# Performance work log

Measured on AMD Instinct MI355X. Metric: run time of the kernel, lower is better.

The kernel has to match this reference:

```python
import jax, jax.numpy as jnp
import numpy as np

T, K, E, D, F = 2048, 6, 32, 2048, 1408   # tokens, top_k, routed experts, dim, moe_inter_dim
S = 2                                      # fused shared experts
C = T * K // E                             # exact per-expert capacity (balanced routing)


def _silu_and_mul(gu):
    # merged gate_up activation: silu(gate_half) * up_half
    g, u = jnp.split(gu, 2, axis=-1)
    return jax.nn.silu(g) * u


def setup_inputs() -> dict:
    key = jax.random.key(0)
    ks = jax.random.split(key, 7)
    x = jax.random.normal(ks[0], (T, D), dtype=jnp.float32)
    # balanced routing: every expert receives exactly C = T*K/E token-expert pairs
    indices = jax.random.permutation(ks[1], jnp.arange(T * K, dtype=jnp.int32) % E).reshape(T, K)
    weights = jax.random.uniform(ks[2], (T, K), dtype=jnp.float32)
    scale = 0.02
    w_gate_up = jax.random.normal(ks[3], (E, D, 2 * F), dtype=jnp.float32) * scale
    w_down = jax.random.normal(ks[4], (E, F, D), dtype=jnp.float32) * scale
    w_gate_up_shared = jax.random.normal(ks[5], (S, D, 2 * F), dtype=jnp.float32) * scale
    w_down_shared = jax.random.normal(ks[6], (S, F, D), dtype=jnp.float32) * scale
    return {"x": x, "weights": weights, "w_gate_up": w_gate_up, "w_down": w_down,
            "w_gate_up_shared": w_gate_up_shared, "w_down_shared": w_down_shared,
            "indices": indices}


def reference(x, weights, w_gate_up, w_down, w_gate_up_shared, w_down_shared, indices):
    # ---- dispatch: sort token-expert pairs by expert id (balanced -> exactly C per expert)
    flat_e = indices.reshape(-1)                       # [T*K]
    order = jnp.argsort(flat_e, stable=True)           # [T*K] pair ids grouped by expert
    tok = order // K                                   # source token of each sorted pair
    w_sorted = weights.reshape(-1)[order]              # routing weight of each sorted pair
    xg = x[tok].reshape(E, C, D)                       # gathered per-expert inputs
    # ---- routed experts: grouped gate_up GEMM -> silu_and_mul -> down GEMM
    act = _silu_and_mul(jnp.einsum('ecd,edf->ecf', xg, w_gate_up))   # [E, C, F]
    down = jnp.einsum('ecf,efd->ecd', act, w_down)                   # [E, C, D]
    # ---- combine: weighted scatter-add back to token order (y[idx] += out * weights[idx, top])
    y = jnp.zeros_like(x).at[tok].add(down.reshape(E * C, D) * w_sorted[:, None])
    # ---- fused shared experts: run on all tokens, added unweighted
    act_s = _silu_and_mul(jnp.einsum('td,sdf->stf', x, w_gate_up_shared))  # [S, T, F]
    y = y + jnp.einsum('stf,sfd->td', act_s, w_down_shared)
    return y
```

## Files before the change

kernel.cpp:

```cpp
#include <hip/hip_runtime.h>
#include <hip/hip_bf16.h>

#define TT 2048
#define KK 6
#define EE 32
#define DD 2048
#define FF 1408
#define SS 2
#define CC 384

typedef __bf16 bf16_t;
typedef __attribute__((ext_vector_type(8))) __bf16 bf16x8;
typedef __attribute__((ext_vector_type(4))) float f32x4;
typedef unsigned int u32;

#define AS1 __attribute__((address_space(1)))
#define AS3 __attribute__((address_space(3)))

__device__ __forceinline__ u32 f2bf(float f) {
    u32 u = __builtin_bit_cast(u32, f);
    return (u + 0x7fffu + ((u >> 16) & 1u)) >> 16;
}
__device__ __forceinline__ u32 pack2(float a, float b) {
    return f2bf(a) | (f2bf(b) << 16);
}
__device__ __forceinline__ float silu_mul(float g, float u) {
    return (g / (1.0f + __expf(-g))) * u;
}

__global__ void k_dispatch(const int* __restrict__ idx, int* __restrict__ counts,
                           int* __restrict__ tok, int* __restrict__ sop) {
    int p = blockIdx.x * 256 + threadIdx.x;
    if (p >= TT * KK) return;
    int e = idx[p];
    int pos = atomicAdd(&counts[e], 1);
    int slot = e * CC + pos;
    tok[slot] = p / KK;
    sop[p] = slot;
}

__global__ void k_gather(const float* __restrict__ x, const int* __restrict__ tok,
                         bf16_t* __restrict__ xall) {
    int row = blockIdx.x;
    int srow = (row < EE * CC) ? tok[row] : (row - EE * CC);
    const float* src = x + (size_t)srow * DD;
    bf16_t* dst = xall + (size_t)row * DD;
    int c0 = threadIdx.x * 8;
    float4 a = *(const float4*)(src + c0);
    float4 b = *(const float4*)(src + c0 + 4);
    uint4 o;
    o.x = pack2(a.x, a.y); o.y = pack2(a.z, a.w);
    o.z = pack2(b.x, b.y); o.w = pack2(b.z, b.w);
    *(uint4*)(dst + c0) = o;
}

#define BSR 44
template<bool FUSED>
__global__ __launch_bounds__(512, 4) void k_gemm_r(
    const bf16_t* __restrict__ Aall, const float* __restrict__ Br,
    bf16_t* __restrict__ Out, int Kdim, int Bstr, int Ostr, int NB)
{
    const int lin = blockIdx.x;
    const int xcd = lin & 7, jj = lin >> 3;
    const int e = xcd + 8 * (jj / NB);
    const int nblk = jj % NB;

    const bf16_t* A = Aall + (size_t)e * CC * Kdim;
    const float* Bbase = Br + (size_t)e * Kdim * Bstr;

    const int tid = threadIdx.x;
    const int lane = tid & 63, wid = tid >> 6;
    const int m_base = wid * 48;
    const int l15 = lane & 15, lq = lane >> 4;
    const int arow = tid >> 2, ac = tid & 3;
    const int bn = tid & 63, kq = tid >> 6;

    const float* bsrc;
    bf16_t* Cout;
    if (FUSED) {
        bsrc = Bbase + ((bn & 32) ? FF : 0) + nblk * 32 + (bn & 31);
        Cout = Out + (size_t)e * CC * Ostr + nblk * 32;
    } else {
        bsrc = Bbase + nblk * 64 + bn;
        Cout = Out + (size_t)e * CC * Ostr + nblk * 64;
    }

    __shared__ __align__(16) bf16_t As[2][384 * 32];
    __shared__ __align__(16) bf16_t Bs[2][64 * BSR];

    f32x4 acc[3][4] = {};
    const int ks = Kdim >> 5;

    auto stageA = [&](int kt, bf16_t* dst) {
        const int k0 = kt << 5;
        #pragma unroll
        for (int i = 0; i < 3; ++i) {
            const int row = i * 128 + arow;
            const int c = ac ^ (arow & 3);
            const bf16_t* g = A + (size_t)row * Kdim + (k0 + c * 8);
            AS3 u32* l = (AS3 u32*)(void*)(dst + (size_t)(i * 128 + wid * 16) * 32);
            __builtin_amdgcn_global_load_lds((const AS1 u32*)(const void*)g, l, 16, 0, 0);
        }
    };
    auto loadB = [&](int kt, float* v) {
        const float* sp = bsrc + (size_t)((kt << 5) + kq * 4) * Bstr;
        #pragma unroll
        for (int t = 0; t < 4; ++t) v[t] = sp[(size_t)t * Bstr];
    };
    auto writeB = [&](bf16_t* bbuf, const float* v) {
        uint2 w;
        w.x = pack2(v[0], v[1]); w.y = pack2(v[2], v[3]);
        *(uint2*)(bbuf + (size_t)bn * BSR + kq * 4) = w;
    };
    auto compute = [&](const bf16_t* abuf, const bf16_t* bbuf) {
        __builtin_amdgcn_s_setprio(1);
        bf16x8 bfr[4];
        #pragma unroll
        for (int j = 0; j < 4; ++j) {
            const int n_ds = FUSED ? ((j & 1) * 16 + (j >> 1) * 32) : (j * 16);
            bfr[j] = *(const bf16x8*)(bbuf + (size_t)(n_ds + l15) * BSR + lq * 8);
        }
        #pragma unroll
        for (int m = 0; m < 3; ++m) {
            const int row = m_base + m * 16 + l15;
            bf16x8 af = *(const bf16x8*)(abuf + (size_t)row * 32
                           + (size_t)((lq ^ (row & 3)) * 8));
            #pragma unroll
            for (int j = 0; j < 4; ++j)
                acc[m][j] = __builtin_amdgcn_mfma_f32_16x16x32_bf16(af, bfr[j], acc[m][j], 0, 0, 0);
        }
        __builtin_amdgcn_s_setprio(0);
    };

    float r0[4], r1[4], r2[4], r3[4];
    bf16_t* const As0 = &As[0][0];  bf16_t* const As1 = &As[1][0];
    bf16_t* const Bs0 = &Bs[0][0];  bf16_t* const Bs1 = &Bs[1][0];

    loadB(0, r0);
    asm volatile("s_waitcnt vmcnt(0)" ::: "memory");
    writeB(Bs0, r0);
    loadB(1, r1);
    loadB(2, r2);
    stageA(0, As0);
    loadB(3, r3);

#define R_ITER(T, RLOAD, RWRITE, ASC, ASN, BSC, BSN)                      \
    {                                                                     \
        const int tb = ((T) + 4 < ks) ? (T) + 4 : ks - 1;                 \
        loadB(tb, RLOAD);                                                 \
        asm volatile("s_waitcnt vmcnt(8)" ::: "memory");                  \
        asm volatile("s_waitcnt lgkmcnt(0)" ::: "memory");                \
        __builtin_amdgcn_s_barrier();                                     \
        const int tn = ((T) + 1 < ks) ? (T) + 1 : ks - 1;                 \
        stageA(tn, ASN);                                                  \
        compute(ASC, BSC);                                                \
        writeB(BSN, RWRITE);                                              \
    }

    for (int t = 0; t < ks; t += 4) {
        R_ITER(t + 0, r0, r1, As0, As1, Bs0, Bs1);
        R_ITER(t + 1, r1, r2, As1, As0, Bs1, Bs0);
        R_ITER(t + 2, r2, r3, As0, As1, Bs0, Bs1);
        R_ITER(t + 3, r3, r0, As1, As0, Bs1, Bs0);
    }
#undef R_ITER

    if (FUSED) {
        #pragma unroll
        for (int m = 0; m < 3; ++m)
            #pragma unroll
            for (int j = 0; j < 2; ++j) {
                const int n = j * 16 + l15;
                #pragma unroll
                for (int rr = 0; rr < 4; ++rr) {
                    const int mm = m_base + m * 16 + lq * 4 + rr;
                    Cout[(size_t)mm * Ostr + n] = (bf16_t)silu_mul(acc[m][j][rr], acc[m][j + 2][rr]);
                }
            }
    } else {
        #pragma unroll
        for (int m = 0; m < 3; ++m)
            #pragma unroll
            for (int j = 0; j < 4; ++j) {
                const int n = j * 16 + l15;
                #pragma unroll
                for (int rr = 0; rr < 4; ++rr) {
                    const int mm = m_base + m * 16 + lq * 4 + rr;
                    Cout[(size_t)mm * Ostr + n] = (bf16_t)acc[m][j][rr];
                }
            }
    }
}

#define BSTR 40
template<bool FUSED>
__global__ __launch_bounds__(256) void k_gemm_s(
    const bf16_t* __restrict__ Ash, const float* __restrict__ Bsh,
    bf16_t* __restrict__ Out, int Kdim, int Bstr, int Ostr, int ash_stride,
    int nkeys, int KQ, int NBs)
{
    const int b = blockIdx.x;
    const int xcd = b & 7, jj = b >> 3;
    const int m = jj / KQ, kqi = jj % KQ;
    const int key = kqi * 8 + xcd;
    if (key >= nkeys) return;
    const int s = key / NBs, nb = key % NBs;

    const bf16_t* A = Ash + ((size_t)s * ash_stride + (size_t)m * 128) * Kdim;
    const float* Bp = Bsh + (size_t)s * Kdim * Bstr;

    const int tid = threadIdx.x;
    const int lane = tid & 63, wid = tid >> 6;
    const int m_off = (wid >> 1) * 64, wn = wid & 1;
    const int l15 = lane & 15, lq = lane >> 4;
    const int arow = tid >> 2, ac = tid & 3;
    const int bn = tid & 127, kh = tid >> 7;

    const float* bsrc;
    bf16_t* Cout;
    if (FUSED) {
        bsrc = Bp + ((bn & 64) ? FF : 0) + nb * 64 + (bn & 63);
        Cout = Out + ((size_t)s * TT + (size_t)m * 128) * Ostr + nb * 64;
    } else {
        bsrc = Bp + nb * 128 + bn;
        Cout = Out + ((size_t)s * TT + (size_t)m * 128) * Ostr + nb * 128;
    }

    __shared__ __align__(16) bf16_t As[2][128 * 32];
    __shared__ __align__(16) bf16_t Bs[2][128 * BSTR];

    f32x4 acc[4][4] = {};
    const int ks = Kdim >> 5;

    auto stageA = [&](int kt, bf16_t* dst) {
        const int k0 = kt << 5;
        #pragma unroll
        for (int i = 0; i < 2; ++i) {
            const int row = i * 64 + arow;
            const int c = ac ^ (arow & 3);
            const bf16_t* g = A + (size_t)row * Kdim + (k0 + c * 8);
            AS3 u32* l = (AS3 u32*)(void*)(dst + (size_t)(i * 64 + wid * 16) * 32);
            __builtin_amdgcn_global_load_lds((const AS1 u32*)(const void*)g, l, 16, 0, 0);
        }
    };
    auto loadB = [&](int kt, float* v) {
        const float* sp = bsrc + (size_t)((kt << 5) + kh * 16) * Bstr;
        #pragma unroll
        for (int t = 0; t < 16; ++t) v[t] = sp[(size_t)t * Bstr];
    };
    auto writeB = [&](bf16_t* bbuf, const float* v) {
        u32 p[8];
        #pragma unroll
        for (int t = 0; t < 8; ++t) p[t] = pack2(v[2 * t], v[2 * t + 1]);
        uint4 w0, w1;
        w0.x = p[0]; w0.y = p[1]; w0.z = p[2]; w0.w = p[3];
        w1.x = p[4]; w1.y = p[5]; w1.z = p[6]; w1.w = p[7];
        *(uint4*)(bbuf + (size_t)bn * BSTR + kh * 16) = w0;
        *(uint4*)(bbuf + (size_t)bn * BSTR + kh * 16 + 8) = w1;
    };
    auto compute = [&](const bf16_t* abuf, const bf16_t* bbuf) {
        bf16x8 af[4], bfr[4];
        #pragma unroll
        for (int i = 0; i < 4; ++i) {
            const int row = m_off + i * 16 + l15;
            af[i] = *(const bf16x8*)(abuf + (size_t)row * 32
                       + (size_t)((lq ^ (row & 3)) * 8));
        }
        #pragma unroll
        for (int j = 0; j < 4; ++j) {
            const int n_ds = FUSED ? (wn * 32 + (j & 1) * 16 + (j >> 1) * 64)
                                   : (wn * 64 + j * 16);
            bfr[j] = *(const bf16x8*)(bbuf + (size_t)(n_ds + l15) * BSTR + lq * 8);
        }
        #pragma unroll
        for (int i = 0; i < 4; ++i)
            #pragma unroll
            for (int j = 0; j < 4; ++j)
                acc[i][j] = __builtin_amdgcn_mfma_f32_16x16x32_bf16(af[i], bfr[j], acc[i][j], 0, 0, 0);
    };

    float r0[16], r1[16], r2[16], r3[16];
    bf16_t* const As0 = &As[0][0];  bf16_t* const As1 = &As[1][0];
    bf16_t* const Bs0 = &Bs[0][0];  bf16_t* const Bs1 = &Bs[1][0];

    loadB(0, r0);
    asm volatile("s_waitcnt vmcnt(0)" ::: "memory");
    writeB(Bs0, r0);
    loadB(1, r1);
    loadB(2, r2);
    stageA(0, As0);
    loadB(3, r3);

#define S_ITER(T, RLOAD, RWRITE, ASC, ASN, BSC, BSN)                      \
    {                                                                     \
        const int tb = ((T) + 4 < ks) ? (T) + 4 : ks - 1;                 \
        loadB(tb, RLOAD);                                                 \
        asm volatile("s_waitcnt vmcnt(32)" ::: "memory");                 \
        asm volatile("s_waitcnt lgkmcnt(0)" ::: "memory");                \
        __builtin_amdgcn_s_barrier();                                     \
        const int tn = ((T) + 1 < ks) ? (T) + 1 : ks - 1;                 \
        stageA(tn, ASN);                                                  \
        compute(ASC, BSC);                                                \
        writeB(BSN, RWRITE);                                              \
    }

    for (int t = 0; t < ks; t += 4) {
        S_ITER(t + 0, r0, r1, As0, As1, Bs0, Bs1);
        S_ITER(t + 1, r1, r2, As1, As0, Bs1, Bs0);
        S_ITER(t + 2, r2, r3, As0, As1, Bs0, Bs1);
        S_ITER(t + 3, r3, r0, As1, As0, Bs1, Bs0);
    }
#undef S_ITER

    if (FUSED) {
        #pragma unroll
        for (int i = 0; i < 4; ++i)
            #pragma unroll
            for (int j = 0; j < 2; ++j) {
                const int n = wn * 32 + j * 16 + l15;
                #pragma unroll
                for (int rr = 0; rr < 4; ++rr) {
                    const int mm = m_off + i * 16 + lq * 4 + rr;
                    Cout[(size_t)mm * Ostr + n] = (bf16_t)silu_mul(acc[i][j][rr], acc[i][j + 2][rr]);
                }
            }
    } else {
        #pragma unroll
        for (int i = 0; i < 4; ++i)
            #pragma unroll
            for (int j = 0; j < 4; ++j) {
                const int n = wn * 64 + j * 16 + l15;
                #pragma unroll
                for (int rr = 0; rr < 4; ++rr) {
                    const int mm = m_off + i * 16 + lq * 4 + rr;
                    Cout[(size_t)mm * Ostr + n] = (bf16_t)acc[i][j][rr];
                }
            }
    }
}

__global__ void k_combine(const bf16_t* __restrict__ down, const int* __restrict__ sop,
                          const float* __restrict__ wts, float* __restrict__ y) {
    int t = blockIdx.x;
    int d0 = threadIdx.x * 8;
    float a[8] = {0, 0, 0, 0, 0, 0, 0, 0};
    #pragma unroll
    for (int k = 0; k < KK; ++k) {
        int slot = sop[t * KK + k];
        float w = wts[t * KK + k];
        bf16x8 v = *(const bf16x8*)(down + (size_t)slot * DD + d0);
        #pragma unroll
        for (int j = 0; j < 8; ++j) a[j] += w * (float)v[j];
    }
    #pragma unroll
    for (int s = 0; s < SS; ++s) {
        bf16x8 v = *(const bf16x8*)(down + ((size_t)EE * CC + (size_t)s * TT + t) * DD + d0);
        #pragma unroll
        for (int j = 0; j < 8; ++j) a[j] += (float)v[j];
    }
    float4 o0, o1;
    o0.x = a[0]; o0.y = a[1]; o0.z = a[2]; o0.w = a[3];
    o1.x = a[4]; o1.y = a[5]; o1.z = a[6]; o1.w = a[7];
    *(float4*)(y + (size_t)t * DD + d0) = o0;
    *(float4*)(y + (size_t)t * DD + d0 + 4) = o1;
}

extern "C" void kernel_launch(void* const* d_in, const int* in_sizes, int n_in,
                              void* d_out, int out_size, void* d_ws, size_t ws_size,
                              hipStream_t stream) {
    (void)in_sizes; (void)n_in; (void)out_size; (void)ws_size;
    const float* x      = (const float*)d_in[0];
    const float* wts    = (const float*)d_in[1];
    const float* w_gu   = (const float*)d_in[2];
    const float* w_dn   = (const float*)d_in[3];
    const float* w_gu_s = (const float*)d_in[4];
    const float* w_dn_s = (const float*)d_in[5];
    const int*   indices= (const int*)d_in[6];
    float* y = (float*)d_out;

    char* ws = (char*)d_ws;
    size_t off = 0;
    auto alloc = [&](size_t bytes) {
        void* p = ws + off;
        off = (off + bytes + 255) & ~(size_t)255;
        return p;
    };
    int*    counts = (int*)alloc((size_t)EE * 4);
    int*    tok    = (int*)alloc((size_t)EE * CC * 4);
    int*    sop    = (int*)alloc((size_t)TT * KK * 4);
    bf16_t* xall   = (bf16_t*)alloc((size_t)(EE * CC + TT) * DD * 2);
    bf16_t* actb   = (bf16_t*)alloc((size_t)(EE * CC + SS * TT) * FF * 2);
    bf16_t* dnout  = (bf16_t*)alloc((size_t)(EE * CC + SS * TT) * DD * 2);

    hipMemsetAsync(counts, 0, EE * 4, stream);
    k_dispatch<<<(TT * KK + 255) / 256, 256, 0, stream>>>(indices, counts, tok, sop);
    k_gather<<<EE * CC + TT, 256, 0, stream>>>(x, tok, xall);

    k_gemm_r<true><<<EE * 44, 512, 0, stream>>>(xall, w_gu, actb, DD, 2 * FF, FF, 44);
    k_gemm_s<true><<<8 * 6 * 16, 256, 0, stream>>>(
        xall + (size_t)EE * CC * DD, w_gu_s, actb + (size_t)EE * CC * FF,
        DD, 2 * FF, FF, 0, 44, 6, 22);

    k_gemm_r<false><<<EE * 32, 512, 0, stream>>>(actb, w_dn, dnout, FF, DD, DD, 32);
    k_gemm_s<false><<<8 * 4 * 16, 256, 0, stream>>>(
        actb + (size_t)EE * CC * FF, w_dn_s, dnout + (size_t)EE * CC * DD,
        FF, DD, DD, TT, 32, 4, 16);

    k_combine<<<TT, 256, 0, stream>>>(dnout, sop, wts, y);
}
```

Baseline: 1.833 ms.

## Simplify routed GEMM: direct global A loads, smaller N tile, 256-thread blocks

```diff
diff --git a/kernel.cpp b/kernel.cpp
--- a/kernel.cpp
+++ b/kernel.cpp
@@ -54,9 +54,8 @@
     *(uint4*)(dst + c0) = o;
 }
 
-#define BSR 44
 template<bool FUSED>
-__global__ __launch_bounds__(512, 4) void k_gemm_r(
+__global__ __launch_bounds__(256, 4) void k_gemm_r(
     const bf16_t* __restrict__ Aall, const float* __restrict__ Br,
     bf16_t* __restrict__ Out, int Kdim, int Bstr, int Ostr, int NB)
 {
@@ -70,118 +69,75 @@
 
     const int tid = threadIdx.x;
     const int lane = tid & 63, wid = tid >> 6;
-    const int m_base = wid * 48;
+    const int m_base = wid * 96;
     const int l15 = lane & 15, lq = lane >> 4;
-    const int arow = tid >> 2, ac = tid & 3;
-    const int bn = tid & 63, kq = tid >> 6;
+    const int bn = tid & 31, kr = tid >> 5;
 
     const float* bsrc;
     bf16_t* Cout;
     if (FUSED) {
-        bsrc = Bbase + ((bn & 32) ? FF : 0) + nblk * 32 + (bn & 31);
+        bsrc = Bbase + ((bn & 16) ? FF : 0) + nblk * 16 + (bn & 15);
+        Cout = Out + (size_t)e * CC * Ostr + nblk * 16;
+    } else {
+        bsrc = Bbase + nblk * 32 + bn;
         Cout = Out + (size_t)e * CC * Ostr + nblk * 32;
-    } else {
-        bsrc = Bbase + nblk * 64 + bn;
-        Cout = Out + (size_t)e * CC * Ostr + nblk * 64;
-    }
-
-    __shared__ __align__(16) bf16_t As[2][384 * 32];
-    __shared__ __align__(16) bf16_t Bs[2][64 * BSR];
-
-    f32x4 acc[3][4] = {};
+    }
+
+    __shared__ __align__(16) bf16_t Bs[2][32 * 36];
+
+    f32x4 acc[6][2] = {};
     const int ks = Kdim >> 5;
 
-    auto stageA = [&](int kt, bf16_t* dst) {
-        const int k0 = kt << 5;
-        #pragma unroll
-        for (int i = 0; i < 3; ++i) {
-            const int row = i * 128 + arow;
-            const int c = ac ^ (arow & 3);
-            const bf16_t* g = A + (size_t)row * Kdim + (k0 + c * 8);
-            AS3 u32* l = (AS3 u32*)(void*)(dst + (size_t)(i * 128 + wid * 16) * 32);
-            __builtin_amdgcn_global_load_lds((const AS1 u32*)(const void*)g, l, 16, 0, 0);
-        }
-    };
-    auto loadB = [&](int kt, float* v) {
-        const float* sp = bsrc + (size_t)((kt << 5) + kq * 4) * Bstr;
+    float v[4];
+    auto loadB = [&](int kt) {
+        const float* sp = bsrc + (size_t)(kt * 32 + kr * 4) * Bstr;
         #pragma unroll
         for (int t = 0; t < 4; ++t) v[t] = sp[(size_t)t * Bstr];
     };
-    auto writeB = [&](bf16_t* bbuf, const float* v) {
+    auto writeB = [&](bf16_t* bbuf) {
         uint2 w;
         w.x = pack2(v[0], v[1]); w.y = pack2(v[2], v[3]);
-        *(uint2*)(bbuf + (size_t)bn * BSR + kq * 4) = w;
-    };
-    auto compute = [&](const bf16_t* abuf, const bf16_t* bbuf) {
-        __builtin_amdgcn_s_setprio(1);
-        bf16x8 bfr[4];
-        #pragma unroll
-        for (int j = 0; j < 4; ++j) {
-            const int n_ds = FUSED ? ((j & 1) * 16 + (j >> 1) * 32) : (j * 16);
-            bfr[j] = *(const bf16x8*)(bbuf + (size_t)(n_ds + l15) * BSR + lq * 8);
-        }
-        #pragma unroll
-        for (int m = 0; m < 3; ++m) {
-            const int row = m_base + m * 16 + l15;
-            bf16x8 af = *(const bf16x8*)(abuf + (size_t)row * 32
-                           + (size_t)((lq ^ (row & 3)) * 8));
-            #pragma unroll
-            for (int j = 0; j < 4; ++j)
+        *(uint2*)(bbuf + bn * 36 + kr * 4) = w;
+    };
+    auto compute = [&](const bf16_t* bbuf, int k0) {
+        bf16x8 bfr[2];
+        #pragma unroll
+        for (int j = 0; j < 2; ++j)
+            bfr[j] = *(const bf16x8*)(bbuf + (j * 16 + l15) * 36 + lq * 8);
+        #pragma unroll
+        for (int m = 0; m < 6; ++m) {
+            const bf16x8 af = *(const bf16x8*)(A
+                + (size_t)(m_base + m * 16 + l15) * Kdim + k0 + lq * 8);
+            #pragma unroll
+            for (int j = 0; j < 2; ++j)
                 acc[m][j] = __builtin_amdgcn_mfma_f32_16x16x32_bf16(af, bfr[j], acc[m][j], 0, 0, 0);
         }
-        __builtin_amdgcn_s_setprio(0);
-    };
-
-    float r0[4], r1[4], r2[4], r3[4];
-    bf16_t* const As0 = &As[0][0];  bf16_t* const As1 = &As[1][0];
-    bf16_t* const Bs0 = &Bs[0][0];  bf16_t* const Bs1 = &Bs[1][0];
-
-    loadB(0, r0);
-    asm volatile("s_waitcnt vmcnt(0)" ::: "memory");
-    writeB(Bs0, r0);
-    loadB(1, r1);
-    loadB(2, r2);
-    stageA(0, As0);
-    loadB(3, r3);
-
-#define R_ITER(T, RLOAD, RWRITE, ASC, ASN, BSC, BSN)                      \
-    {                                                                     \
-        const int tb = ((T) + 4 < ks) ? (T) + 4 : ks - 1;                 \
-        loadB(tb, RLOAD);                                                 \
-        asm volatile("s_waitcnt vmcnt(8)" ::: "memory");                  \
-        asm volatile("s_waitcnt lgkmcnt(0)" ::: "memory");                \
-        __builtin_amdgcn_s_barrier();                                     \
-        const int tn = ((T) + 1 < ks) ? (T) + 1 : ks - 1;                 \
-        stageA(tn, ASN);                                                  \
-        compute(ASC, BSC);                                                \
-        writeB(BSN, RWRITE);                                              \
-    }
-
-    for (int t = 0; t < ks; t += 4) {
-        R_ITER(t + 0, r0, r1, As0, As1, Bs0, Bs1);
-        R_ITER(t + 1, r1, r2, As1, As0, Bs1, Bs0);
-        R_ITER(t + 2, r2, r3, As0, As1, Bs0, Bs1);
-        R_ITER(t + 3, r3, r0, As1, As0, Bs1, Bs0);
-    }
-#undef R_ITER
+    };
+
+    loadB(0);
+    writeB(&Bs[0][0]);
+    __syncthreads();
+    for (int t = 0; t < ks; ++t) {
+        if (t + 1 < ks) loadB(t + 1);
+        compute(&Bs[t & 1][0], t << 5);
+        if (t + 1 < ks) writeB(&Bs[(t + 1) & 1][0]);
+        __syncthreads();
+    }
 
     if (FUSED) {
         #pragma unroll
-        for (int m = 0; m < 3; ++m)
-            #pragma unroll
-            for (int j = 0; j < 2; ++j) {
-                const int n = j * 16 + l15;
-                #pragma unroll
-                for (int rr = 0; rr < 4; ++rr) {
-                    const int mm = m_base + m * 16 + lq * 4 + rr;
-                    Cout[(size_t)mm * Ostr + n] = (bf16_t)silu_mul(acc[m][j][rr], acc[m][j + 2][rr]);
-                }
+        for (int m = 0; m < 6; ++m)
+            #pragma unroll
+            for (int rr = 0; rr < 4; ++rr) {
+                const int mm = m_base + m * 16 + lq * 4 + rr;
+                Cout[(size_t)mm * Ostr + l15] =
+                    (bf16_t)silu_mul(acc[m][0][rr], acc[m][1][rr]);
             }
     } else {
         #pragma unroll
-        for (int m = 0; m < 3; ++m)
-            #pragma unroll
-            for (int j = 0; j < 4; ++j) {
+        for (int m = 0; m < 6; ++m)
+            #pragma unroll
+            for (int j = 0; j < 2; ++j) {
                 const int n = j * 16 + l15;
                 #pragma unroll
                 for (int rr = 0; rr < 4; ++rr) {
@@ -396,12 +352,12 @@
     k_dispatch<<<(TT * KK + 255) / 256, 256, 0, stream>>>(indices, counts, tok, sop);
     k_gather<<<EE * CC + TT, 256, 0, stream>>>(x, tok, xall);
 
-    k_gemm_r<true><<<EE * 44, 512, 0, stream>>>(xall, w_gu, actb, DD, 2 * FF, FF, 44);
+    k_gemm_r<true><<<EE * 88, 256, 0, stream>>>(xall, w_gu, actb, DD, 2 * FF, FF, 88);
     k_gemm_s<true><<<8 * 6 * 16, 256, 0, stream>>>(
         xall + (size_t)EE * CC * DD, w_gu_s, actb + (size_t)EE * CC * FF,
         DD, 2 * FF, FF, 0, 44, 6, 22);
 
-    k_gemm_r<false><<<EE * 32, 512, 0, stream>>>(actb, w_dn, dnout, FF, DD, DD, 32);
+    k_gemm_r<false><<<EE * 64, 256, 0, stream>>>(actb, w_dn, dnout, FF, DD, DD, 64);
     k_gemm_s<false><<<8 * 4 * 16, 256, 0, stream>>>(
         actb + (size_t)EE * CC * FF, w_dn_s, dnout + (size_t)EE * CC * DD,
         FF, DD, DD, TT, 32, 4, 16);
```

Measured after the change: 2.179 ms. 1.19x slower.
